# Performance work log

Measured on AMD Instinct MI355X. Metric: run time of the kernel, lower is better.

Reference implementation:

```python
import jax, jax.numpy as jnp
import numpy as np

B, S, H, DH, E = 8, 2048, 1024, 4096, 8
ALPHA = 0.5
LN_EPS = 1e-5


def setup_inputs() -> dict:
    key = jax.random.key(0)
    ks = jax.random.split(key, 8)
    sc = 0.02
    return {
        "x": jax.random.normal(ks[0], (B, S, H), jnp.float32),
        "We1": jax.random.normal(ks[1], (E, H, DH), jnp.float32) * sc,
        "be1": jnp.zeros((E, DH), jnp.float32),
        "We2": jax.random.normal(ks[2], (E, DH, H), jnp.float32) * sc,
        "be2": jnp.zeros((E, H), jnp.float32),
        "Wq": jax.random.normal(ks[3], (H, H), jnp.float32) * sc,
        "bq": jnp.zeros((H,), jnp.float32),
        "Wk": jax.random.normal(ks[4], (H, H), jnp.float32) * sc,
        "bk": jnp.zeros((H,), jnp.float32),
        "Wv": jax.random.normal(ks[5], (H, H), jnp.float32) * sc,
        "bv": jnp.zeros((H,), jnp.float32),
        "ln_g": jnp.ones((H,), jnp.float32),
        "ln_b": jnp.zeros((H,), jnp.float32),
        "current_expert_idx": E - 1,
    }


def _boosting_forward(x, We1, be1, We2, be2, Wq, bq, Wk, bk, Wv, bv, ln_g, ln_b, cur):
    sg = jax.lax.stop_gradient
    n = cur + 1  # static Python int: number of experts executed
    boost = sg(x)  # boost_input = x.detach()
    outs = []
    for i in range(n):
        h = jax.nn.relu(jnp.einsum("bsh,hf->bsf", boost, We1[i]) + be1[i])
        eo = jnp.einsum("bsf,fh->bsh", h, We2[i]) + be2[i]  # dropout = identity (eval)
        if i < n - 1:
            eo = sg(eo)  # earlier experts detached
        boost = boost + ALPHA * eo
        outs.append(eo)
    stacked = jnp.stack(outs, axis=2)  # [B,S,n,H]
    q = jnp.einsum("bsh,hd->bsd", x, Wq) + bq          # [B,S,H]
    k = jnp.einsum("bseh,hd->bsed", stacked, Wk) + bk  # [B,S,n,H]
    v = jnp.einsum("bseh,hd->bsed", stacked, Wv) + bv
    scores = jnp.einsum("bsd,bsed->bse", q, k) / jnp.sqrt(jnp.asarray(H, x.dtype))
    w = jax.nn.softmax(scores, axis=-1)                # [B,S,n]
    fused = jnp.einsum("bse,bsed->bsd", w, v)          # [B,S,H]
    y = x + fused
    mu = jnp.mean(y, axis=-1, keepdims=True)
    var = jnp.mean(jnp.square(y - mu), axis=-1, keepdims=True)
    return (y - mu) * jax.lax.rsqrt(var + LN_EPS) * ln_g + ln_b


def reference(x, We1, be1, We2, be2, Wq, bq, Wk, bk, Wv, bv, ln_g, ln_b, current_expert_idx):
    return _boosting_forward(x, We1, be1, We2, be2, Wq, bq, Wk, bk, Wv, bv, ln_g, ln_b, int(current_expert_idx))
```

## Files before the change

### kernel.cpp

```cpp
#include <hip/hip_runtime.h>
#include <math.h>

typedef __bf16 bf16_t;
typedef __bf16 bf16x8 __attribute__((ext_vector_type(8)));
typedef __bf16 bf16x4 __attribute__((ext_vector_type(4)));
typedef float f32x4 __attribute__((ext_vector_type(4)));
typedef unsigned int u32;

static constexpr int kBd = 8, kS = 2048, kH = 1024, kDH = 4096, kE = 8;
static constexpr int kM = kBd * kS;
static constexpr float kScale = 0.03125f;

__device__ __forceinline__ void gload_lds16(const void* g, void* l) {
  __builtin_amdgcn_global_load_lds(
      (const __attribute__((address_space(1))) u32*)g,
      (__attribute__((address_space(3))) u32*)l, 16, 0, 0);
}

__global__ __launch_bounds__(256) void cvt_flat_kernel(const float* __restrict__ in,
                                                       bf16_t* __restrict__ out, int n4) {
  int i = blockIdx.x * 256 + threadIdx.x;
  if (i >= n4) return;
  f32x4 v = *(const f32x4*)(in + (size_t)i * 4);
  bf16x4 o;
#pragma unroll
  for (int j = 0; j < 4; ++j) o[j] = (bf16_t)v[j];
  *(bf16x4*)(out + (size_t)i * 4) = o;
}

__global__ __launch_bounds__(256) void transpose_cvt_kernel(
    const float* __restrict__ in, bf16_t* __restrict__ out, int R, int C) {
  __shared__ float tile[32][33];
  int tx = threadIdx.x & 31, ty = threadIdx.x >> 5;
  int c0 = blockIdx.x * 32, r0 = blockIdx.y * 32;
#pragma unroll
  for (int yy = 0; yy < 4; ++yy)
    tile[ty + yy * 8][tx] = in[(size_t)(r0 + ty + yy * 8) * C + c0 + tx];
  __syncthreads();
#pragma unroll
  for (int yy = 0; yy < 4; ++yy)
    out[(size_t)(c0 + ty + yy * 8) * R + r0 + tx] = (bf16_t)tile[tx][ty + yy * 8];
}

template <int MODE>
__global__ __launch_bounds__(512, 2) void gemm256_kernel(
    const bf16_t* __restrict__ A, const bf16_t* __restrict__ Bt,
    int M, int N, int K, int nwg,
    const float* __restrict__ bias,
    bf16_t* __restrict__ outb,
    const float* __restrict__ bin_f, float* __restrict__ bout_f,
    const bf16_t* __restrict__ bin_b, bf16_t* __restrict__ bout_b,
    bf16_t* __restrict__ stacked,
    const float* __restrict__ xres, float* __restrict__ yout,
    const int* __restrict__ curp, int expert_i) {
  if ((MODE == 0 || MODE == 1 || MODE == 4) && expert_i > *curp) return;
  extern __shared__ char lds_buf[];
  char* Abase = lds_buf;
  char* Bbase = lds_buf + 98304;
  const int tid = threadIdx.x;
  const int lane = tid & 63, wid = tid >> 6;
  const int wr = wid >> 2, wc = wid & 3;
  const int fr = lane & 15, fh = lane >> 4;
  const int lane_swz = (fr * 64 + fh * 16) ^ ((fr >> 3) << 5);
  const int bid = blockIdx.x;
  const int wg = (bid & 7) * (nwg >> 3) + (bid >> 3);
  const int nMb = M >> 8;
  const int m0 = (wg % nMb) << 8, n0 = (wg / nMb) << 8;
  int grow[2], gcol[2];
#pragma unroll
  for (int j = 0; j < 2; ++j) {
    int L = (j * 512 + tid) * 16;
    int Lp = L ^ (((L >> 9) & 1) << 5);
    int s = Lp >> 10;
    grow[j] = ((s >> 1) << 4) + ((Lp >> 6) & 15);
    gcol[j] = ((s & 1) << 5) + (((Lp >> 4) & 3) << 3);
  }
  const bf16_t* sA[2] = {A + (size_t)(m0 + grow[0]) * K + gcol[0],
                         A + (size_t)(m0 + grow[1]) * K + gcol[1]};
  const bf16_t* sB[2] = {Bt + (size_t)(n0 + grow[0]) * K + gcol[0],
                         Bt + (size_t)(n0 + grow[1]) * K + gcol[1]};
  const size_t rstep = (size_t)128 * K;

#define STAGE(SP, BASE, tau, h)                                               \
  {                                                                           \
    char* d_ = (BASE) + ((h) << 14) + (wid << 10);                            \
    gload_lds16(SP[0] + (size_t)(h)*rstep + (size_t)(tau)*64, d_);            \
    gload_lds16(SP[1] + (size_t)(h)*rstep + (size_t)(tau)*64, d_ + 8192);     \
  }
#define PIN_VMEM() __builtin_amdgcn_sched_barrier(0x38F)

  const int aoff = (wr << 14) + lane_swz;
  const int boff = ((wc >> 1) << 14) + lane_swz;
  const int bq = (wc & 1) * 4;

  f32x4 acc[8][4] = {};
  const int NT = K >> 6;
  STAGE(sA, Abase, 0, 0); STAGE(sA, Abase, 0, 1);
  STAGE(sB, Bbase, 0, 0); STAGE(sB, Bbase, 0, 1);
  STAGE(sA, Abase + 32768, 1, 0); STAGE(sA, Abase + 32768, 1, 1);
  asm volatile("s_waitcnt vmcnt(4)" ::: "memory");
  __builtin_amdgcn_s_barrier();

  int am = 0, am2 = 2;
  for (int t = 0; t < NT; ++t) {
    const char* Ar = Abase + am * 32768 + aoff;
    const char* Br = Bbase + (t & 1) * 32768 + boff;
    char* stB = Bbase + ((t + 1) & 1) * 32768;
    char* stA = Abase + am2 * 32768;
    bf16x8 b[4][2];
    bf16x8 a0_, a1_, a2_, a3_;

#define RD_A(p)                                                                \
  a0_ = *(const bf16x8*)(Ar + ((2 * (p)) * 2 + 0) * 1024);                     \
  a1_ = *(const bf16x8*)(Ar + ((2 * (p)) * 2 + 1) * 1024);                     \
  a2_ = *(const bf16x8*)(Ar + ((2 * (p) + 1) * 2 + 0) * 1024);                 \
  a3_ = *(const bf16x8*)(Ar + ((2 * (p) + 1) * 2 + 1) * 1024);

#define PH_MFMA(p)                                                             \
  __builtin_amdgcn_s_setprio(1);                                               \
  _Pragma("unroll") for (int nf = 0; nf < 4; ++nf) {                           \
    acc[2 * (p)][nf] =                                                         \
        __builtin_amdgcn_mfma_f32_16x16x32_bf16(a0_, b[nf][0], acc[2 * (p)][nf], 0, 0, 0); \
    acc[2 * (p)][nf] =                                                         \
        __builtin_amdgcn_mfma_f32_16x16x32_bf16(a1_, b[nf][1], acc[2 * (p)][nf], 0, 0, 0); \
    acc[2 * (p) + 1][nf] =                                                     \
        __builtin_amdgcn_mfma_f32_16x16x32_bf16(a2_, b[nf][0], acc[2 * (p) + 1][nf], 0, 0, 0); \
    acc[2 * (p) + 1][nf] =                                                     \
        __builtin_amdgcn_mfma_f32_16x16x32_bf16(a3_, b[nf][1], acc[2 * (p) + 1][nf], 0, 0, 0); \
  }                                                                            \
  __builtin_amdgcn_s_setprio(0);

#pragma unroll
    for (int nf = 0; nf < 4; ++nf)
#pragma unroll
      for (int kk = 0; kk < 2; ++kk)
        b[nf][kk] = *(const bf16x8*)(Br + ((bq + nf) * 2 + kk) * 1024);
    if (t + 1 < NT) { STAGE(sB, stB, t + 1, 0); STAGE(sB, stB, t + 1, 1); }
    PIN_VMEM();
    RD_A(0);
    PH_MFMA(0);
    RD_A(1);
    if (t + 2 < NT) STAGE(sA, stA, t + 2, 0);
    PIN_VMEM();
    PH_MFMA(1);
    RD_A(2);
    if (t + 2 < NT) STAGE(sA, stA, t + 2, 1);
    PIN_VMEM();
    PH_MFMA(2);
    RD_A(3);
    PH_MFMA(3);
    if (t + 2 < NT) {
      asm volatile("s_waitcnt vmcnt(4)" ::: "memory");
    } else {
      asm volatile("s_waitcnt vmcnt(0)" ::: "memory");
    }
    __builtin_amdgcn_s_barrier();
    am = (am == 2) ? 0 : am + 1;
    am2 = (am2 == 2) ? 0 : am2 + 1;
  }
#undef STAGE
#undef PIN_VMEM
#undef PH_MFMA
#undef RD_A

#pragma unroll
  for (int nf = 0; nf < 4; ++nf) {
    const int col = n0 + wc * 64 + nf * 16 + fr;
    const float bv = bias ? bias[col] : 0.0f;
#pragma unroll
    for (int mf = 0; mf < 8; ++mf) {
#pragma unroll
      for (int r = 0; r < 4; ++r) {
        const int row = m0 + wr * 128 + mf * 16 + fh * 4 + r;
        const size_t idx = (size_t)row * N + col;
        float v = acc[mf][nf][r] + bv;
        if (MODE == 0) {
          outb[idx] = (bf16_t)(v > 0.0f ? v : 0.0f);
        } else if (MODE == 2) {
          outb[idx] = (bf16_t)v;
        } else if (MODE == 1) {
          float nb2 = bin_f[idx] + 0.5f * v;
          bout_f[idx] = nb2;
          bout_b[idx] = (bf16_t)nb2;
          stacked[idx] = (bf16_t)v;
        } else if (MODE == 4) {
          float nb2 = (float)bin_b[idx] + 0.5f * v;
          bout_b[idx] = (bf16_t)nb2;
          stacked[idx] = (bf16_t)v;
        } else {
          yout[idx] = v + xres[idx];
        }
      }
    }
  }
}

__global__ __launch_bounds__(256) void scores_mix_kernel(
    const bf16_t* __restrict__ qk, const bf16_t* __restrict__ q,
    const float* __restrict__ bk, const bf16_t* __restrict__ stacked,
    bf16_t* __restrict__ mix, const int* __restrict__ curp) {
  const int n = *curp + 1;
  int lane = threadIdx.x & 63, wave = threadIdx.x >> 6;
  int m = blockIdx.x * 4 + wave;
  size_t base = (size_t)m * kH + lane * 16;
  int c0 = lane * 16;
  bf16x8 qk0 = *(const bf16x8*)(qk + base);
  bf16x8 qk1 = *(const bf16x8*)(qk + base + 8);
  bf16x8 q0 = *(const bf16x8*)(q + base);
  bf16x8 q1 = *(const bf16x8*)(q + base + 8);
  float sc[kE + 1];
  bf16x8 eo0[kE], eo1[kE];
#pragma unroll
  for (int e = 0; e < kE; ++e) {
    sc[e] = 0.0f;
    if (e < n) {
      size_t sb = (size_t)e * kM * kH + base;
      eo0[e] = *(const bf16x8*)(stacked + sb);
      eo1[e] = *(const bf16x8*)(stacked + sb + 8);
      float d = 0.0f;
#pragma unroll
      for (int j = 0; j < 8; ++j)
        d += (float)eo0[e][j] * (float)qk0[j] + (float)eo1[e][j] * (float)qk1[j];
      sc[e] = d;
    }
  }
  {
    float qb = 0.0f;
#pragma unroll
    for (int j = 0; j < 8; ++j)
      qb += (float)q0[j] * bk[c0 + j] + (float)q1[j] * bk[c0 + 8 + j];
    sc[kE] = qb;
  }
#pragma unroll
  for (int off = 32; off >= 1; off >>= 1)
#pragma unroll
    for (int e = 0; e <= kE; ++e) sc[e] += __shfl_xor(sc[e], off, 64);
  float s[kE];
  float mx = -1e30f;
#pragma unroll
  for (int e = 0; e < kE; ++e)
    if (e < n) {
      s[e] = (sc[e] + sc[kE]) * kScale;
      mx = fmaxf(mx, s[e]);
    }
  float Z = 0.0f;
#pragma unroll
  for (int e = 0; e < kE; ++e)
    if (e < n) {
      s[e] = expf(s[e] - mx);
      Z += s[e];
    }
  float inv = 1.0f / Z;
  float mv[16];
#pragma unroll
  for (int j = 0; j < 16; ++j) mv[j] = 0.0f;
#pragma unroll
  for (int e = 0; e < kE; ++e)
    if (e < n) {
      float w = s[e] * inv;
#pragma unroll
      for (int j = 0; j < 8; ++j) {
        mv[j] += w * (float)eo0[e][j];
        mv[8 + j] += w * (float)eo1[e][j];
      }
    }
  bf16x8 o0, o1;
#pragma unroll
  for (int j = 0; j < 8; ++j) {
    o0[j] = (bf16_t)mv[j];
    o1[j] = (bf16_t)mv[8 + j];
  }
  *(bf16x8*)(mix + base) = o0;
  *(bf16x8*)(mix + base + 8) = o1;
}

__global__ __launch_bounds__(256) void layernorm_kernel(
    const float* __restrict__ y, const float* __restrict__ g,
    const float* __restrict__ b, float* __restrict__ out) {
  int lane = threadIdx.x & 63, wave = threadIdx.x >> 6;
  int m = blockIdx.x * 4 + wave;
  size_t base = (size_t)m * kH + lane * 16;
  f32x4 v[4];
#pragma unroll
  for (int j = 0; j < 4; ++j) v[j] = *(const f32x4*)(y + base + j * 4);
  float s = 0.0f, s2 = 0.0f;
#pragma unroll
  for (int j = 0; j < 4; ++j)
#pragma unroll
    for (int t = 0; t < 4; ++t) {
      float u = v[j][t];
      s += u;
      s2 += u * u;
    }
#pragma unroll
  for (int off = 32; off >= 1; off >>= 1) {
    s += __shfl_xor(s, off, 64);
    s2 += __shfl_xor(s2, off, 64);
  }
  float mu = s * (1.0f / kH);
  float var = s2 * (1.0f / kH) - mu * mu;
  float rs = rsqrtf(var + 1e-5f);
  int c0 = lane * 16;
#pragma unroll
  for (int j = 0; j < 4; ++j) {
    f32x4 gg = *(const f32x4*)(g + c0 + j * 4);
    f32x4 bb = *(const f32x4*)(b + c0 + j * 4);
    f32x4 o;
#pragma unroll
    for (int t = 0; t < 4; ++t) o[t] = (v[j][t] - mu) * rs * gg[t] + bb[t];
    *(f32x4*)(out + base + j * 4) = o;
  }
}

extern "C" void kernel_launch(void* const* d_in, const int* in_sizes, int n_in,
                              void* d_out, int out_size, void* d_ws, size_t ws_size,
                              hipStream_t stream) {
  const float* x = (const float*)d_in[0];
  const float* We1 = (const float*)d_in[1];
  const float* be1 = (const float*)d_in[2];
  const float* We2 = (const float*)d_in[3];
  const float* be2 = (const float*)d_in[4];
  const float* Wq = (const float*)d_in[5];
  const float* bq = (const float*)d_in[6];
  const float* Wk = (const float*)d_in[7];
  const float* bk = (const float*)d_in[8];
  const float* Wv = (const float*)d_in[9];
  const float* bv = (const float*)d_in[10];
  const float* ln_g = (const float*)d_in[11];
  const float* ln_b = (const float*)d_in[12];
  const int* curp = (const int*)d_in[13];
  float* out = (float*)d_out;

  char* ws = (char*)d_ws;
  const size_t MB = 1ull << 20;
  bf16_t* stacked = (bf16_t*)(ws);
  bf16_t* xb = (bf16_t*)(ws + 256 * MB);
  bf16_t* boostb = (bf16_t*)(ws + 288 * MB);
  bf16_t* wA = (bf16_t*)(ws + 320 * MB);
  bf16_t* wB = (bf16_t*)(ws + 328 * MB);
  bf16_t* WqT = (bf16_t*)(ws + 336 * MB);
  bf16_t* WkC = (bf16_t*)(ws + 338 * MB);
  bf16_t* WvT = (bf16_t*)(ws + 340 * MB);
  char* dyn = ws + 342 * MB;
  size_t rem = ws_size > 342 * MB ? ws_size - 342 * MB : 0;
  int nchunk;
  bool f32boost;
  if (rem >= 192 * MB) { nchunk = 1; f32boost = true; }
  else if (rem >= 128 * MB) { nchunk = 1; f32boost = false; }
  else if (rem >= 64 * MB) { nchunk = 2; f32boost = false; }
  else { nchunk = 4; f32boost = false; }
  bf16_t* hbuf = (bf16_t*)dyn;
  float* boostf = (float*)(dyn + 128 * MB);
  bf16_t* qb_ = hbuf;
  bf16_t* qkb = boostb;
  bf16_t* mixb = xb;
  float* yf = (float*)ws;

  const int Mc = kM / nchunk;
  const size_t MH = (size_t)kM * kH;
  const u32 kLds = 163840;
  dim3 blk(256), blk5(512);

  cvt_flat_kernel<<<(kM * kH) / 1024, blk, 0, stream>>>(x, xb, (kM * kH) / 4);
  cvt_flat_kernel<<<(kH * kH) / 1024, blk, 0, stream>>>(Wk, WkC, (kH * kH) / 4);
  transpose_cvt_kernel<<<dim3(kH / 32, kH / 32), blk, 0, stream>>>(Wq, WqT, kH, kH);
  transpose_cvt_kernel<<<dim3(kH / 32, kH / 32), blk, 0, stream>>>(Wv, WvT, kH, kH);

  for (int i = 0; i < kE; ++i) {
    transpose_cvt_kernel<<<dim3(kDH / 32, kH / 32), blk, 0, stream>>>(
        We1 + (size_t)i * kH * kDH, wA, kH, kDH);
    transpose_cvt_kernel<<<dim3(kH / 32, kDH / 32), blk, 0, stream>>>(
        We2 + (size_t)i * kH * kDH, wB, kDH, kH);
    for (int c = 0; c < nchunk; ++c) {
      const size_t ro = (size_t)c * Mc * kH;
      const bf16_t* Ain = ((i == 0) ? xb : boostb) + ro;
      {
        int nwg = (Mc / 256) * (kDH / 256);
        gemm256_kernel<0><<<nwg, blk5, kLds, stream>>>(
            Ain, wA, Mc, kDH, kH, nwg, be1 + (size_t)i * kDH, hbuf,
            nullptr, nullptr, nullptr, nullptr, nullptr, nullptr, nullptr, curp, i);
      }
      int nwg = (Mc / 256) * (kH / 256);
      if (f32boost) {
        const float* bin = ((i == 0) ? x : boostf) + ro;
        gemm256_kernel<1><<<nwg, blk5, kLds, stream>>>(
            hbuf, wB, Mc, kH, kDH, nwg, be2 + (size_t)i * kH, nullptr,
            bin, boostf + ro, nullptr, boostb + ro, stacked + (size_t)i * MH + ro,
            nullptr, nullptr, curp, i);
      } else {
        const bf16_t* binb = ((i == 0) ? xb : boostb) + ro;
        gemm256_kernel<4><<<nwg, blk5, kLds, stream>>>(
            hbuf, wB, Mc, kH, kDH, nwg, be2 + (size_t)i * kH, nullptr,
            nullptr, nullptr, binb, boostb + ro, stacked + (size_t)i * MH + ro,
            nullptr, nullptr, curp, i);
      }
    }
  }

  const int nwgH = (kM / 256) * (kH / 256);
  gemm256_kernel<2><<<nwgH, blk5, kLds, stream>>>(
      xb, WqT, kM, kH, kH, nwgH, bq, qb_,
      nullptr, nullptr, nullptr, nullptr, nullptr, nullptr, nullptr, curp, 0);
  gemm256_kernel<2><<<nwgH, blk5, kLds, stream>>>(
      qb_, WkC, kM, kH, kH, nwgH, nullptr, qkb,
      nullptr, nullptr, nullptr, nullptr, nullptr, nullptr, nullptr, curp, 0);
  scores_mix_kernel<<<dim3(kM / 4), blk, 0, stream>>>(qkb, qb_, bk, stacked, mixb, curp);
  gemm256_kernel<3><<<nwgH, blk5, kLds, stream>>>(
      mixb, WvT, kM, kH, kH, nwgH, bv, nullptr,
      nullptr, nullptr, nullptr, nullptr, nullptr, x, yf, curp, 0);
  layernorm_kernel<<<dim3(kM / 4), blk, 0, stream>>>(yf, ln_g, ln_b, out);
}
```

Baseline: 3.089 ms.

## Restructure GEMM main loop into barrier-synchronized 8-phase double-buffered pipeline

Replaces the triple-buffered A / double-buffered B main loop of the 256x256 bf16 GEMM with a double-buffered scheme for both operands. The loop is unrolled by two K-tiles into eight phases, each with explicit LDS reads, a global-to-LDS stage, lgkmcnt waits and workgroup barriers around the MFMA cluster. LDS use drops from 160KB to 128KB per block. The added barriers tighten synchronisation between waves and may cost some overlap, in exchange for more regular interleaving of loads and MFMAs.

```diff
diff --git a/kernel.cpp b/kernel.cpp
--- a/kernel.cpp
+++ b/kernel.cpp
@@ -56,7 +56,7 @@
   if ((MODE == 0 || MODE == 1 || MODE == 4) && expert_i > *curp) return;
   extern __shared__ char lds_buf[];
   char* Abase = lds_buf;
-  char* Bbase = lds_buf + 98304;
+  char* Bbase = lds_buf + 65536;
   const int tid = threadIdx.x;
   const int lane = tid & 63, wid = tid >> 6;
   const int wr = wid >> 2, wc = wid & 3;
@@ -87,81 +87,80 @@
     gload_lds16(SP[0] + (size_t)(h)*rstep + (size_t)(tau)*64, d_);            \
     gload_lds16(SP[1] + (size_t)(h)*rstep + (size_t)(tau)*64, d_ + 8192);     \
   }
-#define PIN_VMEM() __builtin_amdgcn_sched_barrier(0x38F)
-
-  const int aoff = (wr << 14) + lane_swz;
-  const int boff = ((wc >> 1) << 14) + lane_swz;
+#define STAGE_A(t, h) STAGE(sA, Abase + (((t)&1) << 15), (t), (h))
+#define STAGE_B(t, h) STAGE(sB, Bbase + (((t)&1) << 15), (t), (h))
+
   const int bq = (wc & 1) * 4;
 
   f32x4 acc[8][4] = {};
+  bf16x8 b[4][2];
+  bf16x8 a0_, a1_, a2_, a3_;
   const int NT = K >> 6;
-  STAGE(sA, Abase, 0, 0); STAGE(sA, Abase, 0, 1);
-  STAGE(sB, Bbase, 0, 0); STAGE(sB, Bbase, 0, 1);
-  STAGE(sA, Abase + 32768, 1, 0); STAGE(sA, Abase + 32768, 1, 1);
+
+#define PHASE(q, PAR, STG, G)                                                  \
+  {                                                                            \
+    if ((q) == 0) {                                                            \
+      const char* Br = Bbase + (PAR)*32768 + ((wc >> 1) << 14) + lane_swz;     \
+      _Pragma("unroll") for (int nf = 0; nf < 4; ++nf)                         \
+          _Pragma("unroll") for (int kk = 0; kk < 2; ++kk)                     \
+          b[nf][kk] = *(const bf16x8*)(Br + ((bq + nf) * 2 + kk) * 1024);      \
+    }                                                                          \
+    {                                                                          \
+      const char* Ar = Abase + (PAR)*32768 + (wr << 14) + lane_swz;            \
+      a0_ = *(const bf16x8*)(Ar + ((2 * (q)) * 2 + 0) * 1024);                 \
+      a1_ = *(const bf16x8*)(Ar + ((2 * (q)) * 2 + 1) * 1024);                 \
+      a2_ = *(const bf16x8*)(Ar + ((2 * (q) + 1) * 2 + 0) * 1024);             \
+      a3_ = *(const bf16x8*)(Ar + ((2 * (q) + 1) * 2 + 1) * 1024);             \
+    }                                                                          \
+    STG;                                                                       \
+    if ((q) == 0) asm volatile("s_waitcnt lgkmcnt(8)" ::: "memory");           \
+    __builtin_amdgcn_s_barrier();                                              \
+    asm volatile("s_waitcnt lgkmcnt(0)" ::: "memory");                         \
+    __builtin_amdgcn_sched_barrier(0);                                         \
+    __builtin_amdgcn_s_setprio(1);                                             \
+    _Pragma("unroll") for (int nf = 0; nf < 4; ++nf) {                         \
+      acc[2 * (q)][nf] = __builtin_amdgcn_mfma_f32_16x16x32_bf16(              \
+          a0_, b[nf][0], acc[2 * (q)][nf], 0, 0, 0);                           \
+      acc[2 * (q)][nf] = __builtin_amdgcn_mfma_f32_16x16x32_bf16(              \
+          a1_, b[nf][1], acc[2 * (q)][nf], 0, 0, 0);                           \
+      acc[2 * (q) + 1][nf] = __builtin_amdgcn_mfma_f32_16x16x32_bf16(          \
+          a2_, b[nf][0], acc[2 * (q) + 1][nf], 0, 0, 0);                       \
+      acc[2 * (q) + 1][nf] = __builtin_amdgcn_mfma_f32_16x16x32_bf16(          \
+          a3_, b[nf][1], acc[2 * (q) + 1][nf], 0, 0, 0);                       \
+    }                                                                          \
+    __builtin_amdgcn_s_setprio(0);                                             \
+    if ((G) == 1) {                                                            \
+      if (last)                                                                \
+        asm volatile("s_waitcnt vmcnt(0)" ::: "memory");                       \
+      else                                                                     \
+        asm volatile("s_waitcnt vmcnt(4)" ::: "memory");                       \
+    }                                                                          \
+    __builtin_amdgcn_s_barrier();                                              \
+  }
+
+  STAGE_A(0, 0); STAGE_A(0, 1);
+  STAGE_B(0, 0); STAGE_B(0, 1);
+  STAGE_B(1, 0); STAGE_B(1, 1);
   asm volatile("s_waitcnt vmcnt(4)" ::: "memory");
   __builtin_amdgcn_s_barrier();
 
-  int am = 0, am2 = 2;
-  for (int t = 0; t < NT; ++t) {
-    const char* Ar = Abase + am * 32768 + aoff;
-    const char* Br = Bbase + (t & 1) * 32768 + boff;
-    char* stB = Bbase + ((t + 1) & 1) * 32768;
-    char* stA = Abase + am2 * 32768;
-    bf16x8 b[4][2];
-    bf16x8 a0_, a1_, a2_, a3_;
-
-#define RD_A(p)                                                                \
-  a0_ = *(const bf16x8*)(Ar + ((2 * (p)) * 2 + 0) * 1024);                     \
-  a1_ = *(const bf16x8*)(Ar + ((2 * (p)) * 2 + 1) * 1024);                     \
-  a2_ = *(const bf16x8*)(Ar + ((2 * (p) + 1) * 2 + 0) * 1024);                 \
-  a3_ = *(const bf16x8*)(Ar + ((2 * (p) + 1) * 2 + 1) * 1024);
-
-#define PH_MFMA(p)                                                             \
-  __builtin_amdgcn_s_setprio(1);                                               \
-  _Pragma("unroll") for (int nf = 0; nf < 4; ++nf) {                           \
-    acc[2 * (p)][nf] =                                                         \
-        __builtin_amdgcn_mfma_f32_16x16x32_bf16(a0_, b[nf][0], acc[2 * (p)][nf], 0, 0, 0); \
-    acc[2 * (p)][nf] =                                                         \
-        __builtin_amdgcn_mfma_f32_16x16x32_bf16(a1_, b[nf][1], acc[2 * (p)][nf], 0, 0, 0); \
-    acc[2 * (p) + 1][nf] =                                                     \
-        __builtin_amdgcn_mfma_f32_16x16x32_bf16(a2_, b[nf][0], acc[2 * (p) + 1][nf], 0, 0, 0); \
-    acc[2 * (p) + 1][nf] =                                                     \
-        __builtin_amdgcn_mfma_f32_16x16x32_bf16(a3_, b[nf][1], acc[2 * (p) + 1][nf], 0, 0, 0); \
-  }                                                                            \
-  __builtin_amdgcn_s_setprio(0);
-
-#pragma unroll
-    for (int nf = 0; nf < 4; ++nf)
-#pragma unroll
-      for (int kk = 0; kk < 2; ++kk)
-        b[nf][kk] = *(const bf16x8*)(Br + ((bq + nf) * 2 + kk) * 1024);
-    if (t + 1 < NT) { STAGE(sB, stB, t + 1, 0); STAGE(sB, stB, t + 1, 1); }
-    PIN_VMEM();
-    RD_A(0);
-    PH_MFMA(0);
-    RD_A(1);
-    if (t + 2 < NT) STAGE(sA, stA, t + 2, 0);
-    PIN_VMEM();
-    PH_MFMA(1);
-    RD_A(2);
-    if (t + 2 < NT) STAGE(sA, stA, t + 2, 1);
-    PIN_VMEM();
-    PH_MFMA(2);
-    RD_A(3);
-    PH_MFMA(3);
-    if (t + 2 < NT) {
-      asm volatile("s_waitcnt vmcnt(4)" ::: "memory");
-    } else {
-      asm volatile("s_waitcnt vmcnt(0)" ::: "memory");
-    }
-    __builtin_amdgcn_s_barrier();
-    am = (am == 2) ? 0 : am + 1;
-    am2 = (am2 == 2) ? 0 : am2 + 1;
-  }
+  const int nit = NT >> 1;
+  for (int j = 0; j < nit; ++j) {
+    const int t1 = 2 * j + 1, t2 = 2 * j + 2, t3 = 2 * j + 3;
+    const bool last = (j == nit - 1);
+    PHASE(0, 0, STAGE_A(t1, 0), 0);
+    PHASE(1, 0, STAGE_A(t1, 1), 0);
+    PHASE(2, 0, if (t2 < NT) STAGE_B(t2, 0), 0);
+    PHASE(3, 0, if (t2 < NT) STAGE_B(t2, 1), 1);
+    PHASE(0, 1, if (t2 < NT) STAGE_A(t2, 0), 0);
+    PHASE(1, 1, if (t2 < NT) STAGE_A(t2, 1), 0);
+    PHASE(2, 1, if (t3 < NT) STAGE_B(t3, 0), 0);
+    PHASE(3, 1, if (t3 < NT) STAGE_B(t3, 1), 1);
+  }
+#undef PHASE
 #undef STAGE
-#undef PIN_VMEM
-#undef PH_MFMA
-#undef RD_A
+#undef STAGE_A
+#undef STAGE_B
 
 #pragma unroll
   for (int nf = 0; nf < 4; ++nf) {
@@ -358,7 +357,7 @@
 
   const int Mc = kM / nchunk;
   const size_t MH = (size_t)kM * kH;
-  const u32 kLds = 163840;
+  const u32 kLds = 131072;
   dim3 blk(256), blk5(512);
 
   cvt_flat_kernel<<<(kM * kH) / 1024, blk, 0, stream>>>(x, xb, (kM * kH) / 4);
```

New measurement: 3.082 ms. No clear change (-0.2%).

## Deepen B prefetch to two tiles and batch A fragment LDS reads

Applied to the files above, without the earlier changes.

The GEMM main loop now prefetches B tiles two K-steps ahead, matching A, instead of one. A fragments are read from LDS in two batches of eight vectors rather than four per phase. Fine-grained sched barriers and an lgkmcnt wait order the staging against the MFMA phases. The goal is to hide more global-load latency and cut per-phase LDS stalls, at the cost of more registers. There is also a possible race: B for t+2 is written into the same double-buffer slot that other waves may still be reading before the barrier.

```diff
diff --git a/kernel.cpp b/kernel.cpp
--- a/kernel.cpp
+++ b/kernel.cpp
@@ -87,81 +87,78 @@
     gload_lds16(SP[0] + (size_t)(h)*rstep + (size_t)(tau)*64, d_);            \
     gload_lds16(SP[1] + (size_t)(h)*rstep + (size_t)(tau)*64, d_ + 8192);     \
   }
-#define PIN_VMEM() __builtin_amdgcn_sched_barrier(0x38F)
-
-  const int aoff = (wr << 14) + lane_swz;
-  const int boff = ((wc >> 1) << 14) + lane_swz;
+#define STAGE_A(buf, t, h) STAGE(sA, Abase + (buf)*32768, (t), (h))
+#define STAGE_B(t, h) STAGE(sB, Bbase + (((t)&1) << 15), (t), (h))
+#define SB0() __builtin_amdgcn_sched_barrier(0)
+
   const int bq = (wc & 1) * 4;
 
   f32x4 acc[8][4] = {};
   const int NT = K >> 6;
-  STAGE(sA, Abase, 0, 0); STAGE(sA, Abase, 0, 1);
-  STAGE(sB, Bbase, 0, 0); STAGE(sB, Bbase, 0, 1);
-  STAGE(sA, Abase + 32768, 1, 0); STAGE(sA, Abase + 32768, 1, 1);
-  asm volatile("s_waitcnt vmcnt(4)" ::: "memory");
-  __builtin_amdgcn_s_barrier();
-
-  int am = 0, am2 = 2;
-  for (int t = 0; t < NT; ++t) {
-    const char* Ar = Abase + am * 32768 + aoff;
-    const char* Br = Bbase + (t & 1) * 32768 + boff;
-    char* stB = Bbase + ((t + 1) & 1) * 32768;
-    char* stA = Abase + am2 * 32768;
-    bf16x8 b[4][2];
-    bf16x8 a0_, a1_, a2_, a3_;
-
-#define RD_A(p)                                                                \
-  a0_ = *(const bf16x8*)(Ar + ((2 * (p)) * 2 + 0) * 1024);                     \
-  a1_ = *(const bf16x8*)(Ar + ((2 * (p)) * 2 + 1) * 1024);                     \
-  a2_ = *(const bf16x8*)(Ar + ((2 * (p) + 1) * 2 + 0) * 1024);                 \
-  a3_ = *(const bf16x8*)(Ar + ((2 * (p) + 1) * 2 + 1) * 1024);
-
-#define PH_MFMA(p)                                                             \
+
+#define QUAD(p, af)                                                            \
   __builtin_amdgcn_s_setprio(1);                                               \
   _Pragma("unroll") for (int nf = 0; nf < 4; ++nf) {                           \
-    acc[2 * (p)][nf] =                                                         \
-        __builtin_amdgcn_mfma_f32_16x16x32_bf16(a0_, b[nf][0], acc[2 * (p)][nf], 0, 0, 0); \
-    acc[2 * (p)][nf] =                                                         \
-        __builtin_amdgcn_mfma_f32_16x16x32_bf16(a1_, b[nf][1], acc[2 * (p)][nf], 0, 0, 0); \
-    acc[2 * (p) + 1][nf] =                                                     \
-        __builtin_amdgcn_mfma_f32_16x16x32_bf16(a2_, b[nf][0], acc[2 * (p) + 1][nf], 0, 0, 0); \
-    acc[2 * (p) + 1][nf] =                                                     \
-        __builtin_amdgcn_mfma_f32_16x16x32_bf16(a3_, b[nf][1], acc[2 * (p) + 1][nf], 0, 0, 0); \
+    acc[2 * (p)][nf] = __builtin_amdgcn_mfma_f32_16x16x32_bf16(                \
+        af[0], b[nf][0], acc[2 * (p)][nf], 0, 0, 0);                           \
+    acc[2 * (p)][nf] = __builtin_amdgcn_mfma_f32_16x16x32_bf16(                \
+        af[1], b[nf][1], acc[2 * (p)][nf], 0, 0, 0);                           \
+    acc[2 * (p) + 1][nf] = __builtin_amdgcn_mfma_f32_16x16x32_bf16(            \
+        af[2], b[nf][0], acc[2 * (p) + 1][nf], 0, 0, 0);                       \
+    acc[2 * (p) + 1][nf] = __builtin_amdgcn_mfma_f32_16x16x32_bf16(            \
+        af[3], b[nf][1], acc[2 * (p) + 1][nf], 0, 0, 0);                       \
   }                                                                            \
   __builtin_amdgcn_s_setprio(0);
 
+  STAGE_A(0, 0, 0); STAGE_A(0, 0, 1);
+  STAGE_B(0, 0); STAGE_B(0, 1);
+  STAGE_A(1, 1, 0); STAGE_A(1, 1, 1);
+  STAGE_B(1, 0); STAGE_B(1, 1);
+  asm volatile("s_waitcnt vmcnt(8)" ::: "memory");
+  __builtin_amdgcn_s_barrier();
+
+  int am0 = 0;
+  for (int t = 0; t < NT; ++t) {
+    int am2 = am0 + 2; if (am2 >= 3) am2 -= 3;
+    const char* Ar = Abase + am0 * 32768 + (wr << 14) + lane_swz;
+    const char* Br = Bbase + ((t & 1) << 15) + ((wc >> 1) << 14) + lane_swz;
+    bf16x8 b[4][2], a01[8], a23[8];
+    const bool st = (t + 2 < NT);
 #pragma unroll
     for (int nf = 0; nf < 4; ++nf)
 #pragma unroll
       for (int kk = 0; kk < 2; ++kk)
         b[nf][kk] = *(const bf16x8*)(Br + ((bq + nf) * 2 + kk) * 1024);
-    if (t + 1 < NT) { STAGE(sB, stB, t + 1, 0); STAGE(sB, stB, t + 1, 1); }
-    PIN_VMEM();
-    RD_A(0);
-    PH_MFMA(0);
-    RD_A(1);
-    if (t + 2 < NT) STAGE(sA, stA, t + 2, 0);
-    PIN_VMEM();
-    PH_MFMA(1);
-    RD_A(2);
-    if (t + 2 < NT) STAGE(sA, stA, t + 2, 1);
-    PIN_VMEM();
-    PH_MFMA(2);
-    RD_A(3);
-    PH_MFMA(3);
-    if (t + 2 < NT) {
-      asm volatile("s_waitcnt vmcnt(4)" ::: "memory");
+    SB0();
+#pragma unroll
+    for (int i = 0; i < 8; ++i) a01[i] = *(const bf16x8*)(Ar + i * 1024);
+    SB0();
+    if (st) { STAGE_A(am2, t + 2, 0); STAGE_A(am2, t + 2, 1); }
+    SB0();
+    QUAD(0, (&a01[0]));
+#pragma unroll
+    for (int i = 0; i < 8; ++i) a23[i] = *(const bf16x8*)(Ar + (8 + i) * 1024);
+    SB0();
+    QUAD(1, (&a01[4]));
+    asm volatile("s_waitcnt lgkmcnt(8)" ::: "memory");
+    SB0();
+    if (st) { STAGE_B(t + 2, 0); STAGE_B(t + 2, 1); }
+    SB0();
+    QUAD(2, (&a23[0]));
+    QUAD(3, (&a23[4]));
+    if (t < NT - 2) {
+      asm volatile("s_waitcnt vmcnt(8)" ::: "memory");
     } else {
       asm volatile("s_waitcnt vmcnt(0)" ::: "memory");
     }
     __builtin_amdgcn_s_barrier();
-    am = (am == 2) ? 0 : am + 1;
-    am2 = (am2 == 2) ? 0 : am2 + 1;
-  }
+    am0 = am0 + 1; if (am0 >= 3) am0 -= 3;
+  }
+#undef QUAD
 #undef STAGE
-#undef PIN_VMEM
-#undef PH_MFMA
-#undef RD_A
+#undef STAGE_A
+#undef STAGE_B
+#undef SB0
 
 #pragma unroll
   for (int nf = 0; nf < 4; ++nf) {
```

Result: faster. 2.953 ms (-4.4%).
